# Kernel tuning notes

Hardware: AMD Instinct MI355X
Metric: run time of the kernel (lower is better)

## Reference

```python
import jax, jax.numpy as jnp
import numpy as np

D_MODEL = 1024
NHEAD = 16
HEAD_DIM = D_MODEL // NHEAD


def setup_inputs() -> dict:
    key = jax.random.key(0)
    ks = jax.random.split(key, 11)
    B, S = 2, 2048
    s = 1.0 / np.sqrt(D_MODEL)
    return {
        "query": jax.random.normal(ks[0], (B, S, D_MODEL), jnp.float32),
        "key": jax.random.normal(ks[1], (B, S, D_MODEL), jnp.float32),
        "value": jax.random.normal(ks[2], (B, S, D_MODEL), jnp.float32),
        "wq_w": jax.random.normal(ks[3], (D_MODEL, D_MODEL), jnp.float32) * s,
        "wq_b": jax.random.normal(ks[4], (D_MODEL,), jnp.float32) * s,
        "wk_w": jax.random.normal(ks[5], (D_MODEL, D_MODEL), jnp.float32) * s,
        "wk_b": jax.random.normal(ks[6], (D_MODEL,), jnp.float32) * s,
        "wv_w": jax.random.normal(ks[7], (D_MODEL, D_MODEL), jnp.float32) * s,
        "wv_b": jax.random.normal(ks[8], (D_MODEL,), jnp.float32) * s,
        "wo_w": jax.random.normal(ks[9], (D_MODEL, D_MODEL), jnp.float32) * s,
        "wo_b": jax.random.normal(ks[10], (D_MODEL,), jnp.float32) * s,
    }


def reference(query, key, value, wq_w, wq_b, wk_w, wk_b, wv_w, wv_b, wo_w, wo_b):
    B, S, _ = query.shape
    # torch Linear: x @ W.T + b
    def proj(x, w, b):
        y = x @ w.T + b
        return y.reshape(B, S, NHEAD, HEAD_DIM).transpose(0, 2, 1, 3)  # [B,H,S,Dh]

    Q = proj(query, wq_w, wq_b)
    K = proj(key, wk_w, wk_b)
    V = proj(value, wv_w, wv_b)

    scale = 1.0 / np.sqrt(HEAD_DIM).astype(np.float32)
    scores = jnp.einsum("bhqd,bhkd->bhqk", Q, K) * scale  # [B,H,S,S]
    causal = jnp.tril(jnp.ones((S, S), dtype=bool))
    scores = jnp.where(causal, scores, -jnp.inf)
    attn = jax.nn.softmax(scores, axis=-1)
    out = jnp.einsum("bhqk,bhkd->bhqd", attn, V)  # [B,H,S,Dh]
    out = out.transpose(0, 2, 1, 3).reshape(B, S, D_MODEL)
    return out @ wo_w.T + wo_b
```

## Files before the change

kernel.cpp:

```cpp
#include <hip/hip_runtime.h>
#include <stdint.h>

#define D_MODEL 1024
#define S_LEN   2048
#define NHEAD   16
#define HEAD_DIM 64
#define BATCH   2
#define M_TOT   (BATCH * S_LEN)
#define Q_SCALE 0.18033688011112042f

using bf16x8 = __attribute__((ext_vector_type(8))) short;
using f32x4  = __attribute__((ext_vector_type(4))) float;

__device__ __forceinline__ unsigned short f2bf(float f) {
  union { float f; unsigned int u; } v; v.f = f;
  unsigned int u = v.u;
  return (unsigned short)((u + 0x7FFFu + ((u >> 16) & 1u)) >> 16);
}
__device__ __forceinline__ unsigned int pkbf(float a, float b) {
#if __has_builtin(__builtin_amdgcn_cvt_pk_bf16_f32)
  auto p = __builtin_amdgcn_cvt_pk_bf16_f32(a, b);
  union { decltype(p) v; unsigned int u; } c; c.v = p;
  return c.u;
#else
  return (unsigned int)f2bf(a) | ((unsigned int)f2bf(b) << 16);
#endif
}
__device__ __forceinline__ bf16x8 cvt8(const float* p) {
  const float4 a = *(const float4*)p;
  const float4 b = *(const float4*)(p + 4);
  union { unsigned int u[4]; bf16x8 v; } r;
  r.u[0] = pkbf(a.x, a.y); r.u[1] = pkbf(a.z, a.w);
  r.u[2] = pkbf(b.x, b.y); r.u[3] = pkbf(b.z, b.w);
  return r.v;
}
__device__ __forceinline__ float fexp2(float x) {
#if __has_builtin(__builtin_amdgcn_exp2f)
  return __builtin_amdgcn_exp2f(x);
#else
  return __expf(x * 0.69314718055994531f);
#endif
}
__device__ __forceinline__ void async16(const unsigned short* g, short* l) {
  __builtin_amdgcn_global_load_lds(
      reinterpret_cast<const __attribute__((address_space(1))) unsigned int*>(
          reinterpret_cast<uintptr_t>(g)),
      reinterpret_cast<__attribute__((address_space(3))) unsigned int*>(
          reinterpret_cast<uintptr_t>(l)),
      16, 0, 0);
}

__device__ __forceinline__ void swap32(unsigned int& x, unsigned int& y) {
#if __has_builtin(__builtin_amdgcn_permlane32_swap)
  auto r = __builtin_amdgcn_permlane32_swap(x, y, false, false);
  x = (unsigned int)r[0]; y = (unsigned int)r[1];
#else
  const int lane = threadIdx.x & 63;
  unsigned int sx = (unsigned int)__shfl_xor((int)x, 32);
  unsigned int sy = (unsigned int)__shfl_xor((int)y, 32);
  unsigned int nx = (lane & 32) ? sy : x;
  unsigned int ny = (lane & 32) ? y : sx;
  x = nx; y = ny;
#endif
}
__device__ __forceinline__ void swap16(unsigned int& x, unsigned int& y) {
#if __has_builtin(__builtin_amdgcn_permlane16_swap)
  auto r = __builtin_amdgcn_permlane16_swap(x, y, false, false);
  x = (unsigned int)r[0]; y = (unsigned int)r[1];
#else
  const int lane = threadIdx.x & 63;
  unsigned int sx = (unsigned int)__shfl_xor((int)x, 16);
  unsigned int sy = (unsigned int)__shfl_xor((int)y, 16);
  unsigned int nx = (lane & 16) ? sy : x;
  unsigned int ny = (lane & 16) ? y : sx;
  x = nx; y = ny;
#endif
}

#define LDK 40

__global__ __launch_bounds__(256)
void cast_all(const float* __restrict__ wq, const float* __restrict__ wk,
              const float* __restrict__ wv, const float* __restrict__ wo,
              const float* __restrict__ q, const float* __restrict__ k,
              const float* __restrict__ v,
              unsigned short* __restrict__ wb,
              unsigned short* __restrict__ qb, unsigned short* __restrict__ kb,
              unsigned short* __restrict__ vb)
{
  const int z = blockIdx.y;
  const float* src;
  unsigned short* d;
  size_t n;
  switch (z) {
    case 0: src = wq; d = wb;                                   n = (size_t)D_MODEL * D_MODEL; break;
    case 1: src = wk; d = wb + (size_t)1 * D_MODEL * D_MODEL;   n = (size_t)D_MODEL * D_MODEL; break;
    case 2: src = wv; d = wb + (size_t)2 * D_MODEL * D_MODEL;   n = (size_t)D_MODEL * D_MODEL; break;
    case 3: src = wo; d = wb + (size_t)3 * D_MODEL * D_MODEL;   n = (size_t)D_MODEL * D_MODEL; break;
    case 4: src = q;  d = qb;                                   n = (size_t)M_TOT * D_MODEL;   break;
    case 5: src = k;  d = kb;                                   n = (size_t)M_TOT * D_MODEL;   break;
    default: src = v; d = vb;                                   n = (size_t)M_TOT * D_MODEL;   break;
  }
  const size_t i = ((size_t)blockIdx.x * 256 + threadIdx.x) * 8;
  if (i < n) *(bf16x8*)(d + i) = cvt8(src + i);
}

__device__ __forceinline__ void gemm_tile_lds8w(const unsigned short* __restrict__ A,
                                                const unsigned short* __restrict__ W,
                                                int m0, int n0,
                                                short* As, short* Bs,
                                                f32x4 acc[4][2])
{
  const int t    = threadIdx.x;
  const int lane = t & 63;
  const int w    = t >> 6;
  const int quad = lane >> 4;
  const int l16  = lane & 15;
  const int wm   = (w >> 2) * 64;
  const int wn   = (w & 3) * 32;
  const int srow = t >> 2;
  const int scol = (t & 3) * 8;

  for (int mt = 0; mt < 4; ++mt)
    for (int nt = 0; nt < 2; ++nt)
      acc[mt][nt] = f32x4{0.f, 0.f, 0.f, 0.f};

  for (int kt = 0; kt < D_MODEL / 32; ++kt) {
    const int kc = kt * 32 + scol;
    __syncthreads();
    async16(A + (size_t)(m0 + srow) * D_MODEL + kc, As + srow * 32 + scol);
    async16(W + (size_t)(n0 + srow) * D_MODEL + kc, Bs + srow * 32 + scol);
    __syncthreads();

    bf16x8 af[4], bfr[2];
    for (int mt = 0; mt < 4; ++mt)
      af[mt] = *(const bf16x8*)(As + (wm + mt * 16 + l16) * 32 + quad * 8);
    for (int nt = 0; nt < 2; ++nt)
      bfr[nt] = *(const bf16x8*)(Bs + (wn + nt * 16 + l16) * 32 + quad * 8);
    for (int mt = 0; mt < 4; ++mt)
      for (int nt = 0; nt < 2; ++nt)
        acc[mt][nt] = __builtin_amdgcn_mfma_f32_16x16x32_bf16(af[mt], bfr[nt], acc[mt][nt], 0, 0, 0);
  }
}

__device__ __forceinline__ void gemm_tile_lds64(const unsigned short* __restrict__ A,
                                                const unsigned short* __restrict__ W,
                                                int m0, int n0,
                                                short* As, short* Bs,
                                                f32x4 acc[2][4])
{
  const int t    = threadIdx.x;
  const int lane = t & 63;
  const int w    = t >> 6;
  const int quad = lane >> 4;
  const int l16  = lane & 15;
  const int wm   = (w >> 1) * 32;
  const int wn   = (w & 1) * 64;
  const int srow = t >> 2;
  const int scol = (t & 3) * 8;

  for (int mt = 0; mt < 2; ++mt)
    for (int nt = 0; nt < 4; ++nt)
      acc[mt][nt] = f32x4{0.f, 0.f, 0.f, 0.f};

  for (int kt = 0; kt < D_MODEL / 32; ++kt) {
    const int kc = kt * 32 + scol;
    __syncthreads();
    async16(A + (size_t)(m0 + srow)      * D_MODEL + kc, As + srow * 32 + scol);
    async16(W + (size_t)(n0 + srow)      * D_MODEL + kc, Bs + srow * 32 + scol);
    async16(W + (size_t)(n0 + 64 + srow) * D_MODEL + kc, Bs + (64 + srow) * 32 + scol);
    __syncthreads();

    bf16x8 af[2], bfr[4];
    for (int mt = 0; mt < 2; ++mt)
      af[mt] = *(const bf16x8*)(As + (wm + mt * 16 + l16) * 32 + quad * 8);
    for (int nt = 0; nt < 4; ++nt)
      bfr[nt] = *(const bf16x8*)(Bs + (wn + nt * 16 + l16) * 32 + quad * 8);
    for (int mt = 0; mt < 2; ++mt)
      for (int nt = 0; nt < 4; ++nt)
        acc[mt][nt] = __builtin_amdgcn_mfma_f32_16x16x32_bf16(af[mt], bfr[nt], acc[mt][nt], 0, 0, 0);
  }
}

__device__ __forceinline__ void gemm_tile_f32(const float* __restrict__ A,
                                              const unsigned short* __restrict__ W,
                                              int m0, int n0,
                                              short* As, short* Bs,
                                              f32x4 acc[4][4])
{
  const int t    = threadIdx.x;
  const int lane = t & 63;
  const int w    = t >> 6;
  const int quad = lane >> 4;
  const int l16  = lane & 15;
  const int wm   = (w >> 1) * 64;
  const int wn   = (w & 1) * 64;
  const int srow = t >> 2;
  const int scol = (t & 3) * 8;

  for (int mt = 0; mt < 4; ++mt)
    for (int nt = 0; nt < 4; ++nt)
      acc[mt][nt] = f32x4{0.f, 0.f, 0.f, 0.f};

  for (int kt = 0; kt < D_MODEL / 32; ++kt) {
    const int kc = kt * 32 + scol;
    const bf16x8 a0 = cvt8(A + (size_t)(m0 + srow)      * D_MODEL + kc);
    const bf16x8 a1 = cvt8(A + (size_t)(m0 + srow + 64) * D_MODEL + kc);
    const bf16x8 b0 = *(const bf16x8*)(W + (size_t)(n0 + srow)      * D_MODEL + kc);
    const bf16x8 b1 = *(const bf16x8*)(W + (size_t)(n0 + srow + 64) * D_MODEL + kc);
    __syncthreads();
    *(bf16x8*)(As + (srow)      * LDK + scol) = a0;
    *(bf16x8*)(As + (srow + 64) * LDK + scol) = a1;
    *(bf16x8*)(Bs + (srow)      * LDK + scol) = b0;
    *(bf16x8*)(Bs + (srow + 64) * LDK + scol) = b1;
    __syncthreads();

    bf16x8 af[4], bfr[4];
    for (int mt = 0; mt < 4; ++mt)
      af[mt] = *(const bf16x8*)(As + (wm + mt * 16 + l16) * LDK + quad * 8);
    for (int nt = 0; nt < 4; ++nt)
      bfr[nt] = *(const bf16x8*)(Bs + (wn + nt * 16 + l16) * LDK + quad * 8);
    for (int mt = 0; mt < 4; ++mt)
      for (int nt = 0; nt < 4; ++nt)
        acc[mt][nt] = __builtin_amdgcn_mfma_f32_16x16x32_bf16(af[mt], bfr[nt], acc[mt][nt], 0, 0, 0);
  }
}

__device__ __forceinline__ void qkv_epilogue8w(int z, int m0, int n0,
                                               const float* __restrict__ bias,
                                               float scale,
                                               unsigned short* __restrict__ dst,
                                               f32x4 acc[4][2])
{
  const int t    = threadIdx.x;
  const int lane = t & 63;
  const int w    = t >> 6;
  const int quad = lane >> 4;
  const int l16  = lane & 15;
  const int wm   = (w >> 2) * 64;
  const int wn   = (w & 3) * 32;

  for (int nt = 0; nt < 2; ++nt) {
    const int n = n0 + wn + nt * 16 + l16;
    const float bb = bias[n];
    const int h = n >> 6, d = n & 63;
    for (int mt = 0; mt < 4; ++mt) {
      for (int r = 0; r < 4; ++r) {
        const int m = m0 + wm + mt * 16 + quad * 4 + r;
        const int b = m >> 11, s = m & 2047;
        const unsigned short val = f2bf((acc[mt][nt][r] + bb) * scale);
        if (z < 2)
          dst[((size_t)((b * NHEAD + h) * S_LEN + s)) * HEAD_DIM + d] = val;
        else
          dst[((size_t)((b * NHEAD + h) * HEAD_DIM + d)) * S_LEN + s] = val;
      }
    }
  }
}

__global__ __launch_bounds__(512)
void qkv_fast(const unsigned short* __restrict__ qb,
              const unsigned short* __restrict__ kb,
              const unsigned short* __restrict__ vb,
              const unsigned short* __restrict__ wqb,
              const unsigned short* __restrict__ wkb,
              const unsigned short* __restrict__ wvb,
              const float* __restrict__ bq, const float* __restrict__ bk,
              const float* __restrict__ bv,
              unsigned short* __restrict__ Qh, unsigned short* __restrict__ Kh,
              unsigned short* __restrict__ VhT)
{
  __shared__ __attribute__((aligned(16))) short As[128 * 32];
  __shared__ __attribute__((aligned(16))) short Bs[128 * 32];
  const int z = blockIdx.z;
  const unsigned short* A    = (z == 0) ? qb  : (z == 1) ? kb  : vb;
  const unsigned short* W    = (z == 0) ? wqb : (z == 1) ? wkb : wvb;
  const float*          bias = (z == 0) ? bq  : (z == 1) ? bk  : bv;
  unsigned short*       dst  = (z == 0) ? Qh  : (z == 1) ? Kh  : VhT;
  const float           scale = (z == 0) ? Q_SCALE : 1.0f;

  const int m0 = blockIdx.x * 128, n0 = blockIdx.y * 128;
  f32x4 acc[4][2];
  gemm_tile_lds8w(A, W, m0, n0, As, Bs, acc);
  qkv_epilogue8w(z, m0, n0, bias, scale, dst, acc);
}

__global__ __launch_bounds__(256)
void qkv_slow(const float* __restrict__ query, const float* __restrict__ key,
              const float* __restrict__ value,
              const unsigned short* __restrict__ wqb,
              const unsigned short* __restrict__ wkb,
              const unsigned short* __restrict__ wvb,
              const float* __restrict__ bq, const float* __restrict__ bk,
              const float* __restrict__ bv,
              unsigned short* __restrict__ Qh, unsigned short* __restrict__ Kh,
              unsigned short* __restrict__ VhT)
{
  __shared__ __attribute__((aligned(16))) short As[128 * LDK];
  __shared__ __attribute__((aligned(16))) short Bs[128 * LDK];
  const int z = blockIdx.z;
  const float*          A    = (z == 0) ? query : (z == 1) ? key : value;
  const unsigned short* W    = (z == 0) ? wqb   : (z == 1) ? wkb : wvb;
  const float*          bias = (z == 0) ? bq    : (z == 1) ? bk  : bv;
  unsigned short*       dst  = (z == 0) ? Qh    : (z == 1) ? Kh  : VhT;
  const float           scale = (z == 0) ? Q_SCALE : 1.0f;

  const int m0 = blockIdx.x * 128, n0 = blockIdx.y * 128;
  f32x4 acc[4][4];
  gemm_tile_f32(A, W, m0, n0, As, Bs, acc);

  const int t    = threadIdx.x;
  const int lane = t & 63;
  const int w    = t >> 6;
  const int quad = lane >> 4;
  const int l16  = lane & 15;
  const int wm   = (w >> 1) * 64;
  const int wn   = (w & 1) * 64;
  for (int nt = 0; nt < 4; ++nt) {
    const int n = n0 + wn + nt * 16 + l16;
    const float bb = bias[n];
    const int h = n >> 6, d = n & 63;
    for (int mt = 0; mt < 4; ++mt) {
      for (int r = 0; r < 4; ++r) {
        const int m = m0 + wm + mt * 16 + quad * 4 + r;
        const int b = m >> 11, s = m & 2047;
        const unsigned short val = f2bf((acc[mt][nt][r] + bb) * scale);
        if (z < 2)
          dst[((size_t)((b * NHEAD + h) * S_LEN + s)) * HEAD_DIM + d] = val;
        else
          dst[((size_t)((b * NHEAD + h) * HEAD_DIM + d)) * S_LEN + s] = val;
      }
    }
  }
}

__global__ __launch_bounds__(256)
void out_proj(const unsigned short* __restrict__ Oh,
              const unsigned short* __restrict__ wob,
              const float* __restrict__ bo,
              float* __restrict__ dst)
{
  __shared__ __attribute__((aligned(16))) short As[64 * 32];
  __shared__ __attribute__((aligned(16))) short Bs[128 * 32];
  const int m0 = blockIdx.x * 64, n0 = blockIdx.y * 128;
  f32x4 acc[2][4];
  gemm_tile_lds64(Oh, wob, m0, n0, As, Bs, acc);

  const int t    = threadIdx.x;
  const int lane = t & 63;
  const int w    = t >> 6;
  const int quad = lane >> 4;
  const int l16  = lane & 15;
  const int wm   = (w >> 1) * 32;
  const int wn   = (w & 1) * 64;

  for (int nt = 0; nt < 4; ++nt) {
    const int n = n0 + wn + nt * 16 + l16;
    const float bb = bo[n];
    for (int mt = 0; mt < 2; ++mt)
      for (int r = 0; r < 4; ++r) {
        const int m = m0 + wm + mt * 16 + quad * 4 + r;
        dst[(size_t)m * D_MODEL + n] = acc[mt][nt][r] + bb;
      }
  }
}

struct Frags { bf16x8 ka0, ka1, kb0, kb1, v0, v1, v2, v3; };
struct StageRegs { bf16x8 k0, k1, v0, v1; };

#define KS_LD 72
#define VT_LD 136

__device__ __forceinline__ StageRegs load_stage(const unsigned short* __restrict__ Kb,
                                                const unsigned short* __restrict__ Vb,
                                                int k0, int kr, int kc, int vd, int vc) {
  StageRegs r;
  r.k0 = *(const bf16x8*)(Kb + (size_t)(k0 + kr)      * HEAD_DIM + kc);
  r.k1 = *(const bf16x8*)(Kb + (size_t)(k0 + kr + 64) * HEAD_DIM + kc);
  r.v0 = *(const bf16x8*)(Vb + (size_t)(vd)      * S_LEN + k0 + vc);
  r.v1 = *(const bf16x8*)(Vb + (size_t)(vd + 32) * S_LEN + k0 + vc);
  return r;
}
__device__ __forceinline__ void write_stage(const StageRegs& r, short* Ks, short* Vts,
                                            int kr, int kc, int vd, int vc) {
  *(bf16x8*)(Ks + (kr)      * KS_LD + kc) = r.k0;
  *(bf16x8*)(Ks + (kr + 64) * KS_LD + kc) = r.k1;
  *(bf16x8*)(Vts + (vd)      * VT_LD + vc) = r.v0;
  *(bf16x8*)(Vts + (vd + 32) * VT_LD + vc) = r.v1;
}
__device__ __forceinline__ Frags lds_frags(const short* Ks, const short* Vts,
                                           int c, int quad, int l16) {
  Frags f;
  const short* kp = Ks + (c * 32 + l16) * KS_LD + quad * 8;
  f.ka0 = *(const bf16x8*)(kp);
  f.ka1 = *(const bf16x8*)(kp + 32);
  f.kb0 = *(const bf16x8*)(kp + 16 * KS_LD);
  f.kb1 = *(const bf16x8*)(kp + 16 * KS_LD + 32);
  const short* vp = Vts + l16 * VT_LD + c * 32 + quad * 8;
  f.v0 = *(const bf16x8*)(vp);
  f.v1 = *(const bf16x8*)(vp + 16 * VT_LD);
  f.v2 = *(const bf16x8*)(vp + 32 * VT_LD);
  f.v3 = *(const bf16x8*)(vp + 48 * VT_LD);
  return f;
}

template <int MODE>
__device__ __forceinline__ void proc_chunk(const Frags& f, const bf16x8 qf[2],
                                           const bf16x8& ones, int quad, int l16,
                                           f32x4& lacc, f32x4 oacc[4]) {
  f32x4 s0 = f32x4{0.f, 0.f, 0.f, 0.f};
  f32x4 s1 = f32x4{0.f, 0.f, 0.f, 0.f};
  __builtin_amdgcn_s_setprio(1);
  s0 = __builtin_amdgcn_mfma_f32_16x16x32_bf16(f.ka0, qf[0], s0, 0, 0, 0);
  s0 = __builtin_amdgcn_mfma_f32_16x16x32_bf16(f.ka1, qf[1], s0, 0, 0, 0);
  if (MODE != 1) {
    s1 = __builtin_amdgcn_mfma_f32_16x16x32_bf16(f.kb0, qf[0], s1, 0, 0, 0);
    s1 = __builtin_amdgcn_mfma_f32_16x16x32_bf16(f.kb1, qf[1], s1, 0, 0, 0);
  }
  __builtin_amdgcn_s_setprio(0);

  float st0[4], st1[4];
  const int kl = quad * 4;
#pragma unroll
  for (int r = 0; r < 4; ++r) {
    if (MODE == 0) {
      st0[r] = fexp2(s0[r]);
      st1[r] = fexp2(s1[r]);
    } else if (MODE == 1) {
      st0[r] = (kl + r <= l16) ? fexp2(s0[r]) : 0.f;
      st1[r] = 0.f;
    } else {
      st0[r] = fexp2(s0[r]);
      st1[r] = (kl + r <= l16) ? fexp2(s1[r]) : 0.f;
    }
  }

  unsigned int a = pkbf(st0[0], st0[1]), b = pkbf(st0[2], st0[3]);
  unsigned int c = pkbf(st1[0], st1[1]), e = pkbf(st1[2], st1[3]);
  swap32(a, c); swap32(b, e);
  swap16(a, c); swap16(b, e);
  union { unsigned int u[4]; bf16x8 v; } pf;
  pf.u[0] = a; pf.u[1] = b; pf.u[2] = c; pf.u[3] = e;

  __builtin_amdgcn_s_setprio(1);
  lacc = __builtin_amdgcn_mfma_f32_16x16x32_bf16(pf.v, ones, lacc, 0, 0, 0);
  oacc[0] = __builtin_amdgcn_mfma_f32_16x16x32_bf16(pf.v, f.v0, oacc[0], 0, 0, 0);
  oacc[1] = __builtin_amdgcn_mfma_f32_16x16x32_bf16(pf.v, f.v1, oacc[1], 0, 0, 0);
  oacc[2] = __builtin_amdgcn_mfma_f32_16x16x32_bf16(pf.v, f.v2, oacc[2], 0, 0, 0);
  oacc[3] = __builtin_amdgcn_mfma_f32_16x16x32_bf16(pf.v, f.v3, oacc[3], 0, 0, 0);
  __builtin_amdgcn_s_setprio(0);
}

__global__ __launch_bounds__(512, 4)
void attn_kernel(const unsigned short* __restrict__ Qh,
                 const unsigned short* __restrict__ Kh,
                 const unsigned short* __restrict__ VhT,
                 unsigned short* __restrict__ O)
{
  __shared__ __attribute__((aligned(16))) short Ks[2][128 * KS_LD];
  __shared__ __attribute__((aligned(16))) short Vts[2][64 * VT_LD];

  const int orig = blockIdx.x;
  const int xcd  = orig & 7;
  const int li   = orig >> 3;
  const int bh   = xcd * 4 + (li & 3);
  const int qt   = 15 - (li >> 2);
  const int q0   = qt * 128;
  const int b    = bh >> 4;
  const int h    = bh & 15;
  const int t    = threadIdx.x;
  const int w    = t >> 6;
  const int lane = t & 63;
  const int quad = lane >> 4;
  const int l16  = lane & 15;
  const int rowbase = q0 + w * 16;

  const unsigned short* Kb = Kh + (size_t)bh * S_LEN * HEAD_DIM;
  const unsigned short* Vb = VhT + (size_t)bh * HEAD_DIM * S_LEN;
  const int kr = t >> 3, kc = (t & 7) * 8;
  const int vd = t >> 4, vc = (t & 15) * 8;

  bf16x8 qf[2];
  {
    const size_t qrow = (size_t)bh * S_LEN + rowbase + l16;
    qf[0] = *(const bf16x8*)(Qh + qrow * HEAD_DIM + quad * 8);
    qf[1] = *(const bf16x8*)(Qh + qrow * HEAD_DIM + 32 + quad * 8);
  }
  bf16x8 ones;
#pragma unroll
  for (int j = 0; j < 8; ++j) ones[j] = (short)0x3F80;

  f32x4 lacc = f32x4{0.f, 0.f, 0.f, 0.f};
  f32x4 oacc[4];
#pragma unroll
  for (int dt = 0; dt < 4; ++dt) oacc[dt] = f32x4{0.f, 0.f, 0.f, 0.f};

  const int nT = qt + 1;
  const int cw = w >> 1;
  const bool odd = (w & 1) != 0;

  StageRegs rs = load_stage(Kb, Vb, 0, kr, kc, vd, vc);
  write_stage(rs, Ks[0], Vts[0], kr, kc, vd, vc);
  __syncthreads();
  for (int j = 0; j < nT; ++j) {
    const short* Ksj = (j & 1) ? Ks[1] : Ks[0];
    const short* Vtj = (j & 1) ? Vts[1] : Vts[0];
    short* Ksn = (j & 1) ? Ks[0] : Ks[1];
    short* Vtn = (j & 1) ? Vts[0] : Vts[1];
    const bool more = (j + 1 < nT);
    if (more) rs = load_stage(Kb, Vb, (j + 1) * 128, kr, kc, vd, vc);
    if (j < qt) {
#pragma unroll
      for (int c = 0; c < 4; ++c) {
        const Frags f = lds_frags(Ksj, Vtj, c, quad, l16);
        proc_chunk<0>(f, qf, ones, quad, l16, lacc, oacc);
      }
    } else {
      for (int c = 0; c < cw; ++c) {
        const Frags f = lds_frags(Ksj, Vtj, c, quad, l16);
        proc_chunk<0>(f, qf, ones, quad, l16, lacc, oacc);
      }
      const Frags f = lds_frags(Ksj, Vtj, cw, quad, l16);
      if (odd) proc_chunk<2>(f, qf, ones, quad, l16, lacc, oacc);
      else     proc_chunk<1>(f, qf, ones, quad, l16, lacc, oacc);
    }
    if (more) write_stage(rs, Ksn, Vtn, kr, kc, vd, vc);
    __syncthreads();
  }

#pragma unroll
  for (int dt = 0; dt < 4; ++dt)
#pragma unroll
    for (int r = 0; r < 4; ++r) {
      const int rowg = rowbase + quad * 4 + r;
      O[(size_t)(b * S_LEN + rowg) * D_MODEL + h * 64 + dt * 16 + l16] =
          f2bf(oacc[dt][r] / lacc[r]);
    }
}

extern "C" void kernel_launch(void* const* d_in, const int* in_sizes, int n_in,
                              void* d_out, int out_size, void* d_ws, size_t ws_size,
                              hipStream_t stream)
{
  (void)in_sizes; (void)n_in; (void)out_size;
  const float* q  = (const float*)d_in[0];
  const float* k  = (const float*)d_in[1];
  const float* v  = (const float*)d_in[2];
  const float* wq = (const float*)d_in[3];
  const float* bq = (const float*)d_in[4];
  const float* wk = (const float*)d_in[5];
  const float* bk = (const float*)d_in[6];
  const float* wv = (const float*)d_in[7];
  const float* bv = (const float*)d_in[8];
  const float* wo = (const float*)d_in[9];
  const float* bo = (const float*)d_in[10];
  float* out = (float*)d_out;

  unsigned short* wb  = (unsigned short*)d_ws;
  unsigned short* wqb = wb;
  unsigned short* wkb = wb + (size_t)1 * D_MODEL * D_MODEL;
  unsigned short* wvb = wb + (size_t)2 * D_MODEL * D_MODEL;
  unsigned short* wob = wb + (size_t)3 * D_MODEL * D_MODEL;
  unsigned short* Kh  = wb + (size_t)4 * D_MODEL * D_MODEL;
  unsigned short* VhT = Kh + (size_t)M_TOT * D_MODEL;
  unsigned short* Oh  = VhT + (size_t)M_TOT * D_MODEL;
  unsigned short* qb  = Oh;
  unsigned short* vb  = Oh + (size_t)M_TOT * D_MODEL;
  unsigned short* Qh  = (unsigned short*)d_out;
  unsigned short* kb  = Qh + (size_t)M_TOT * D_MODEL;

  const bool fast = ws_size >= (size_t)40 * 1024 * 1024;

  if (fast) {
    dim3 gc((size_t)M_TOT * D_MODEL / (256 * 8), 7, 1);
    cast_all<<<gc, 256, 0, stream>>>(wq, wk, wv, wo, q, k, v, wb, qb, kb, vb);
    dim3 g1(M_TOT / 128, D_MODEL / 128, 3);
    qkv_fast<<<g1, 512, 0, stream>>>(qb, kb, vb, wqb, wkb, wvb, bq, bk, bv, Qh, Kh, VhT);
  } else {
    dim3 gc((size_t)D_MODEL * D_MODEL / (256 * 8), 4, 1);
    cast_all<<<gc, 256, 0, stream>>>(wq, wk, wv, wo, q, k, v, wb, qb, kb, vb);
    dim3 g1(M_TOT / 128, D_MODEL / 128, 3);
    qkv_slow<<<g1, 256, 0, stream>>>(q, k, v, wqb, wkb, wvb, bq, bk, bv, Qh, Kh, VhT);
  }

  dim3 g2(512, 1, 1);
  attn_kernel<<<g2, 512, 0, stream>>>(Qh, Kh, VhT, Oh);

  dim3 g3(M_TOT / 64, D_MODEL / 128, 1);
  out_proj<<<g3, 256, 0, stream>>>(Oh, wob, bo, out);
}
```

Before: 212.6 us.

## Triple-buffer QKV GEMM LDS tiles with async prefetch and one barrier per step

Replaces the QKV projection GEMM's single-buffered K loop, which had two full barriers per step, with a three-stage LDS ring. Global-to-LDS loads run two tiles ahead, guarded by explicit vmcnt waits and a single s_barrier per iteration. MFMA issue is also wrapped in s_setprio to favour matrix work. This overlaps global load latency with compute, at the cost of triple the LDS footprint and hand-placed waitcnt correctness risk.

```diff
diff --git a/kernel.cpp b/kernel.cpp
--- a/kernel.cpp
+++ b/kernel.cpp
@@ -48,6 +48,19 @@
       reinterpret_cast<__attribute__((address_space(3))) unsigned int*>(
           reinterpret_cast<uintptr_t>(l)),
       16, 0, 0);
+}
+
+__device__ __forceinline__ void waitv2() {
+  asm volatile("s_waitcnt vmcnt(2)" ::: "memory");
+  __builtin_amdgcn_sched_barrier(0);
+}
+__device__ __forceinline__ void waitv0() {
+  asm volatile("s_waitcnt vmcnt(0)" ::: "memory");
+  __builtin_amdgcn_sched_barrier(0);
+}
+__device__ __forceinline__ void waitl0() {
+  asm volatile("s_waitcnt lgkmcnt(0)" ::: "memory");
+  __builtin_amdgcn_sched_barrier(0);
 }
 
 __device__ __forceinline__ void swap32(unsigned int& x, unsigned int& y) {
@@ -105,11 +118,13 @@
   if (i < n) *(bf16x8*)(d + i) = cvt8(src + i);
 }
 
-__device__ __forceinline__ void gemm_tile_lds8w(const unsigned short* __restrict__ A,
-                                                const unsigned short* __restrict__ W,
-                                                int m0, int n0,
-                                                short* As, short* Bs,
-                                                f32x4 acc[4][2])
+#define QBUF (128 * 32)
+
+__device__ __forceinline__ void gemm_tile_cv(const unsigned short* __restrict__ A,
+                                             const unsigned short* __restrict__ W,
+                                             int m0, int n0,
+                                             short* As, short* Bs,
+                                             f32x4 acc[4][2])
 {
   const int t    = threadIdx.x;
   const int lane = t & 63;
@@ -120,26 +135,58 @@
   const int wn   = (w & 3) * 32;
   const int srow = t >> 2;
   const int scol = (t & 3) * 8;
+  const int sdst = srow * 32 + scol;
+
+  const unsigned short* Ag = A + (size_t)(m0 + srow) * D_MODEL + scol;
+  const unsigned short* Wg = W + (size_t)(n0 + srow) * D_MODEL + scol;
 
   for (int mt = 0; mt < 4; ++mt)
     for (int nt = 0; nt < 2; ++nt)
       acc[mt][nt] = f32x4{0.f, 0.f, 0.f, 0.f};
 
-  for (int kt = 0; kt < D_MODEL / 32; ++kt) {
-    const int kc = kt * 32 + scol;
-    __syncthreads();
-    async16(A + (size_t)(m0 + srow) * D_MODEL + kc, As + srow * 32 + scol);
-    async16(W + (size_t)(n0 + srow) * D_MODEL + kc, Bs + srow * 32 + scol);
-    __syncthreads();
-
+  async16(Ag,      As + sdst);
+  async16(Wg,      Bs + sdst);
+  async16(Ag + 32, As + QBUF + sdst);
+  async16(Wg + 32, Bs + QBUF + sdst);
+  waitv2();
+  __builtin_amdgcn_s_barrier();
+
+  int rc = 0;
+  for (int kt = 0; kt < 32; ++kt) {
+    const short* ab = As + rc * QBUF;
+    const short* bb = Bs + rc * QBUF;
     bf16x8 af[4], bfr[2];
+#pragma unroll
     for (int mt = 0; mt < 4; ++mt)
-      af[mt] = *(const bf16x8*)(As + (wm + mt * 16 + l16) * 32 + quad * 8);
+      af[mt] = *(const bf16x8*)(ab + (wm + mt * 16 + l16) * 32 + quad * 8);
+#pragma unroll
     for (int nt = 0; nt < 2; ++nt)
-      bfr[nt] = *(const bf16x8*)(Bs + (wn + nt * 16 + l16) * 32 + quad * 8);
+      bfr[nt] = *(const bf16x8*)(bb + (wn + nt * 16 + l16) * 32 + quad * 8);
+
+    const bool more = (kt + 2 < 32);
+    if (more) {
+      const int wcIdx = (rc + 2 >= 3) ? rc - 1 : rc + 2;
+      const int kc = (kt + 2) * 32;
+      async16(Ag + kc, As + wcIdx * QBUF + sdst);
+      async16(Wg + kc, Bs + wcIdx * QBUF + sdst);
+    }
+
+    waitl0();
+
+    __builtin_amdgcn_s_setprio(1);
+#pragma unroll
     for (int mt = 0; mt < 4; ++mt)
+#pragma unroll
       for (int nt = 0; nt < 2; ++nt)
         acc[mt][nt] = __builtin_amdgcn_mfma_f32_16x16x32_bf16(af[mt], bfr[nt], acc[mt][nt], 0, 0, 0);
+    __builtin_amdgcn_s_setprio(0);
+
+    if (kt < 31) {
+      if (more) waitv2();
+      else      waitv0();
+      __builtin_amdgcn_s_barrier();
+    }
+    rc = (rc == 2) ? 0 : rc + 1;
   }
 }
 
@@ -270,8 +317,8 @@
               unsigned short* __restrict__ Qh, unsigned short* __restrict__ Kh,
               unsigned short* __restrict__ VhT)
 {
-  __shared__ __attribute__((aligned(16))) short As[128 * 32];
-  __shared__ __attribute__((aligned(16))) short Bs[128 * 32];
+  __shared__ __attribute__((aligned(16))) short As[3 * QBUF];
+  __shared__ __attribute__((aligned(16))) short Bs[3 * QBUF];
   const int z = blockIdx.z;
   const unsigned short* A    = (z == 0) ? qb  : (z == 1) ? kb  : vb;
   const unsigned short* W    = (z == 0) ? wqb : (z == 1) ? wkb : wvb;
@@ -281,7 +328,7 @@
 
   const int m0 = blockIdx.x * 128, n0 = blockIdx.y * 128;
   f32x4 acc[4][2];
-  gemm_tile_lds8w(A, W, m0, n0, As, Bs, acc);
+  gemm_tile_cv(A, W, m0, n0, As, Bs, acc);
   qkv_epilogue8w(z, m0, n0, bias, scale, dst, acc);
 }
 
```

Result: no change. 213.5 us (+0.4%).
